# Kernel optimization log

Hardware: AMD Instinct MI355X
Metric: run time of the kernel (lower is better)

## Reference

```python
import jax, jax.numpy as jnp
import numpy as np

EMBED_DIM = 1024
B, S = 8, 2048


def setup_inputs() -> dict:
    key = jax.random.key(0)
    ks = jax.random.split(key, 8)
    scale = 1.0 / np.sqrt(EMBED_DIM)
    return {
        "mha_output": jax.random.normal(ks[0], (B, S, EMBED_DIM), dtype=jnp.float32),
        "gates": jax.random.uniform(ks[1], (B, S), dtype=jnp.float32),
        "Wq": jax.random.uniform(ks[2], (EMBED_DIM, EMBED_DIM), jnp.float32, -scale, scale),
        "bq": jax.random.uniform(ks[3], (EMBED_DIM,), jnp.float32, -scale, scale),
        "Wk": jax.random.uniform(ks[4], (EMBED_DIM, EMBED_DIM), jnp.float32, -scale, scale),
        "bk": jax.random.uniform(ks[5], (EMBED_DIM,), jnp.float32, -scale, scale),
        "Wv": jax.random.uniform(ks[6], (EMBED_DIM, EMBED_DIM), jnp.float32, -scale, scale),
        "bv": jax.random.uniform(ks[7], (EMBED_DIM,), jnp.float32, -scale, scale),
    }


def reference(mha_output, gates, Wq, bq, Wk, bk, Wv, bv):
    # gates: (B, S) -> (B, S, 1) for elementwise modulation
    g = gates[..., None]
    # Linear layers (torch convention: x @ W^T + b)
    Q = jnp.einsum('bsd,ed->bse', mha_output, Wq) + bq
    K = jnp.einsum('bsd,ed->bse', mha_output, Wk) + bk
    V = jnp.einsum('bsd,ed->bse', mha_output, Wv) + bv
    Q_mod = Q * g
    K_mod = K * g
    temperature = jnp.sqrt(jnp.asarray(EMBED_DIM, dtype=mha_output.dtype))
    scores = jnp.einsum('bqd,bkd->bqk', Q_mod, K_mod) / temperature  # (B, S, S)
    attn_weights = jax.nn.softmax(scores, axis=-1)
    gated_attn_output = jnp.einsum('bqk,bkd->bqd', attn_weights, V)
    return gated_attn_output, attn_weights
```

## Files before the change

### kernel.cpp

```cpp
#include <hip/hip_runtime.h>

#define SEQ  2048
#define EMB  1024
#define NBAT 8
#define NROW (NBAT*SEQ)

using u16 = unsigned short;
typedef float  f32x4  __attribute__((ext_vector_type(4)));
typedef __bf16 bf16x8 __attribute__((ext_vector_type(8)));
typedef u16    u16x8  __attribute__((ext_vector_type(8)));
typedef u16    u16x4  __attribute__((ext_vector_type(4)));

__device__ __forceinline__ u16 f2bf(float x) {
  unsigned u = __builtin_bit_cast(unsigned, x);
  return (u16)((u + 0x7fffu + ((u >> 16) & 1u)) >> 16);
}
__device__ __forceinline__ float bf2f(u16 h) {
  return __builtin_bit_cast(float, ((unsigned)h) << 16);
}

__device__ __forceinline__ f32x4 mfma16(u16x8 a, u16x8 b, f32x4 c) {
  return __builtin_amdgcn_mfma_f32_16x16x32_bf16(
      __builtin_bit_cast(bf16x8, a), __builtin_bit_cast(bf16x8, b), c, 0, 0, 0);
}

__device__ __forceinline__ void async_cp16(const u16* g, u16* l) {
  __builtin_amdgcn_global_load_lds(
      (const __attribute__((address_space(1))) void*)(g),
      (__attribute__((address_space(3))) void*)(l), 16, 0, 0);
}

__device__ __forceinline__ void stage_half(const u16* __restrict__ g, int ld,
                                           u16* __restrict__ lds, int wid, int lane)
{
  const int lr = lane >> 2;
  const int bb = (lr & 1) ^ ((lr >> 2) & 1);
  const int row16 = (lr & ~1) | bb;
  const int ck = (lane & 3) ^ ((lr & 2) | bb);
#pragma unroll
  for (int l = 0; l < 2; ++l) {
    const int r0 = wid * 32 + l * 16;
    async_cp16(g + (size_t)(r0 + row16) * ld + ck * 8, lds + r0 * 32);
  }
}

__device__ __forceinline__ void ph_reads_A8(const u16* __restrict__ sAh,
                                            int wr, int r, int kg, int xr, u16x8 a[8])
{
#pragma unroll
  for (int i = 0; i < 8; ++i) {
    const int row = wr * 128 + i * 16 + r;
    a[i] = *(const u16x8*)&sAh[(row * 32 + kg * 8) ^ xr];
  }
}
__device__ __forceinline__ void ph_reads_B(const u16* __restrict__ sBh,
                                           int wc, int r, int kg, int xr, u16x8 b[4])
{
#pragma unroll
  for (int j = 0; j < 4; ++j) {
    const int row = wc * 64 + j * 16 + r;
    b[j] = *(const u16x8*)&sBh[(row * 32 + kg * 8) ^ xr];
  }
}

__device__ __forceinline__ void mfma_block8(const u16x8 a[8], const u16x8 b[4],
                                            f32x4 (*accp)[4])
{
#pragma unroll
  for (int i = 0; i < 8; ++i)
#pragma unroll
    for (int j = 0; j < 4; ++j)
      accp[i][j] = mfma16(a[i], b[j], accp[i][j]);
}

#define DECL_LDS_8PH()                                                       \
  __shared__ alignas(16) u16 sAls[2][2][256 * 32];                           \
  __shared__ alignas(16) u16 sBls[2][2][256 * 32]

#define PH2(READS, STAGE, WAIT)                                              \
  READS                                                                      \
  STAGE                                                                      \
  WAIT                                                                       \
  __builtin_amdgcn_s_barrier();                                              \
  asm volatile("s_waitcnt lgkmcnt(0)" ::: "memory");                         \
  __builtin_amdgcn_sched_barrier(0);                                         \
  __builtin_amdgcn_s_setprio(1);                                             \
  mfma_block8(a_, b_, acc);                                                  \
  __builtin_amdgcn_s_setprio(0);                                             \
  __builtin_amdgcn_s_barrier();

#define GEMM_2PH(Aptr, ldA, Bptr, ldB, NTv)                                  \
  {                                                                          \
    const int r_ = lane & 15, kg_ = lane >> 4;                               \
    const int xr_ = (r_ & 7) << 3;                                           \
    stage_half((Aptr),      (ldA), &sAls[0][0][0], wid, lane);               \
    stage_half((Aptr) + 32, (ldA), &sAls[0][1][0], wid, lane);               \
    stage_half((Bptr),      (ldB), &sBls[0][0][0], wid, lane);               \
    stage_half((Bptr) + 32, (ldB), &sBls[0][1][0], wid, lane);               \
    asm volatile("s_waitcnt vmcnt(2)" ::: "memory");                         \
    __builtin_amdgcn_sched_barrier(0);                                       \
    __builtin_amdgcn_s_barrier();                                            \
    u16x8 a_[8], b_[4];                                                      \
    for (int tt = 0; tt < (NTv); ++tt) {                                     \
      const int s_ = tt & 1, s2_ = s_ ^ 1;                                   \
      const u16* A0_ = &sAls[s_][0][0]; const u16* A1_ = &sAls[s_][1][0];    \
      const u16* B0_ = &sBls[s_][0][0]; const u16* B1_ = &sBls[s_][1][0];    \
      const bool pf_ = (tt + 1 < (NTv));                                     \
      PH2({ ph_reads_A8(A0_, wr, r_, kg_, xr_, a_);                          \
            ph_reads_B(B0_, wc, r_, kg_, xr_, b_); },                        \
          { if (pf_) {                                                       \
              stage_half((Aptr) + (tt + 1) * 64,      (ldA),                 \
                         &sAls[s2_][0][0], wid, lane);                       \
              stage_half((Aptr) + (tt + 1) * 64 + 32, (ldA),                 \
                         &sAls[s2_][1][0], wid, lane);                       \
              stage_half((Bptr) + (tt + 1) * 64,      (ldB),                 \
                         &sBls[s2_][0][0], wid, lane);                       \
              stage_half((Bptr) + (tt + 1) * 64 + 32, (ldB),                 \
                         &sBls[s2_][1][0], wid, lane);                       \
            } },                                                             \
          { if (pf_) asm volatile("s_waitcnt vmcnt(8)" ::: "memory");        \
            else     asm volatile("s_waitcnt vmcnt(0)" ::: "memory");        \
            __builtin_amdgcn_sched_barrier(0); })                            \
      PH2({ ph_reads_A8(A1_, wr, r_, kg_, xr_, a_);                          \
            ph_reads_B(B1_, wc, r_, kg_, xr_, b_); },                        \
          { },                                                               \
          { if (pf_) { asm volatile("s_waitcnt vmcnt(2)" ::: "memory");      \
            __builtin_amdgcn_sched_barrier(0); } })                          \
    }                                                                        \
  }

#define DECL_ACC()                                                           \
  f32x4 acc[8][4];                                                           \
  _Pragma("unroll")                                                          \
  for (int i = 0; i < 8; ++i)                                                \
    _Pragma("unroll")                                                        \
    for (int j = 0; j < 4; ++j)                                              \
      _Pragma("unroll")                                                      \
      for (int q = 0; q < 4; ++q) acc[i][j][q] = 0.0f

__device__ __forceinline__ int xcd_swz(int bid, int nwg) {
  return (bid & 7) * (nwg >> 3) + (bid >> 3);
}

__global__ __launch_bounds__(256) void prep_kernel(
    const float* __restrict__ X,
    const float* __restrict__ Wq, const float* __restrict__ Wk, const float* __restrict__ Wv,
    u16* __restrict__ Xb, u16* __restrict__ Wb)
{
  const size_t i = ((size_t)blockIdx.x * 256 + threadIdx.x) * 4;
  const size_t nx = (size_t)NROW * EMB;
  f32x4 v;
  u16* dst;
  if (i < nx) {
    v = *(const f32x4*)(X + i);
    dst = Xb + i;
  } else {
    const size_t j = i - nx;
    const int m = (int)(j / ((size_t)EMB * EMB));
    const size_t o = j - (size_t)m * EMB * EMB;
    const float* W = (m == 0) ? Wq : (m == 1) ? Wk : Wv;
    v = *(const f32x4*)(W + o);
    dst = Wb + j;
  }
  u16x4 h;
#pragma unroll
  for (int j = 0; j < 4; ++j) h[j] = f2bf(v[j]);
  *(u16x4*)dst = h;
}

__global__ __launch_bounds__(512, 2) void proj_kernel(
    const u16* __restrict__ Xb, const u16* __restrict__ Wb,
    const float* __restrict__ bq, const float* __restrict__ bk, const float* __restrict__ bv,
    u16* __restrict__ Qb, u16* __restrict__ Kb, u16* __restrict__ VT)
{
  DECL_LDS_8PH();
  const int nwg = 4 * 64 * 3;
  int wg = xcd_swz(blockIdx.x, nwg);
  const int n0 = (wg & 3) * 256;        wg >>= 2;
  const int m0 = (wg & 63) * 256;       wg >>= 6;
  const int mat = wg;

  const int t = threadIdx.x, lane = t & 63, wid = t >> 6;
  const int wr = wid >> 2, wc = wid & 3;

  const u16* A = Xb + (size_t)m0 * EMB;
  const u16* B = Wb + (size_t)mat * EMB * EMB + (size_t)n0 * EMB;

  DECL_ACC();
  GEMM_2PH(A, EMB, B, EMB, EMB / 64);

  const float* bias = (mat == 0) ? bq : (mat == 1) ? bk : bv;
  const int r = lane & 15, kg = lane >> 4;
#pragma unroll
  for (int i = 0; i < 8; ++i) {
#pragma unroll
    for (int j = 0; j < 4; ++j) {
      const int c = n0 + wc * 64 + j * 16 + r;
      const float bb = bias[c];
      if (mat == 2) {
        const int bi = m0 >> 11;
        const int sbase = (m0 & (SEQ - 1)) + wr * 128 + i * 16 + kg * 4;
        u16x4 hv;
#pragma unroll
        for (int rg = 0; rg < 4; ++rg) hv[rg] = f2bf(acc[i][j][rg] + bb);
        *(u16x4*)&VT[((size_t)bi * EMB + c) * SEQ + sbase] = hv;
      } else {
        u16* D = (mat == 0) ? Qb : Kb;
#pragma unroll
        for (int rg = 0; rg < 4; ++rg) {
          const int row = m0 + wr * 128 + i * 16 + kg * 4 + rg;
          D[(size_t)row * EMB + c] = f2bf(acc[i][j][rg] + bb);
        }
      }
    }
  }
}

__global__ __launch_bounds__(512, 2) void scores_kernel(
    const u16* __restrict__ Qb, const u16* __restrict__ Kb,
    const float* __restrict__ gates, u16* __restrict__ raw)
{
  DECL_LDS_8PH();
  const int nwg = 8 * 8 * NBAT;
  int wg = xcd_swz(blockIdx.x, nwg);
  const int n0 = (wg & 7) * 256;        wg >>= 3;
  const int q0 = (wg & 7) * 256;        wg >>= 3;
  const int b  = wg;

  const int t = threadIdx.x, lane = t & 63, wid = t >> 6;
  const int wr = wid >> 2, wc = wid & 3;

  const u16* A = Qb + ((size_t)b * SEQ + q0) * EMB;
  const u16* B = Kb + ((size_t)b * SEQ + n0) * EMB;

  DECL_ACC();
  GEMM_2PH(A, EMB, B, EMB, EMB / 64);

  const float* gb = gates + (size_t)b * SEQ;
  u16* rawB = raw + ((size_t)b * SEQ + q0) * SEQ;
  const int r = lane & 15, kg = lane >> 4;

  float gkj[4];
#pragma unroll
  for (int j = 0; j < 4; ++j) gkj[j] = gb[n0 + wc * 64 + j * 16 + r] * 0.03125f;

#pragma unroll
  for (int i = 0; i < 8; ++i) {
#pragma unroll
    for (int rg = 0; rg < 4; ++rg) {
      const int qr = wr * 128 + i * 16 + kg * 4 + rg;
      const float gq = gb[q0 + qr];
#pragma unroll
      for (int j = 0; j < 4; ++j) {
        const int col = n0 + wc * 64 + j * 16 + r;
        rawB[(size_t)qr * SEQ + col] = f2bf(expf(acc[i][j][rg] * gq * gkj[j]));
      }
    }
  }
}

__global__ __launch_bounds__(256) void rownorm_kernel(
    const u16* __restrict__ raw, float* __restrict__ attn, float* __restrict__ invl)
{
  const int row = blockIdx.x;
  const int t = threadIdx.x, lane = t & 63, wid = t >> 6;
  const u16* rp = raw + (size_t)row * SEQ + t * 8;
  u16x8 h = *(const u16x8*)rp;
  float e[8];
  float s = 0.f;
#pragma unroll
  for (int j = 0; j < 8; ++j) { e[j] = bf2f(h[j]); s += e[j]; }
#pragma unroll
  for (int off = 32; off >= 1; off >>= 1) s += __shfl_xor(s, off);
  __shared__ float red[4];
  if (lane == 0) red[wid] = s;
  __syncthreads();
  s = (red[0] + red[1]) + (red[2] + red[3]);
  const float iv = 1.0f / s;
  float* ap = attn + (size_t)row * SEQ + t * 8;
  f32x4 w0, w1;
#pragma unroll
  for (int j = 0; j < 4; ++j) { w0[j] = e[j] * iv; w1[j] = e[j + 4] * iv; }
  *(f32x4*)ap       = w0;
  *(f32x4*)(ap + 4) = w1;
  if (t == 0) invl[row] = iv;
}

__global__ __launch_bounds__(512, 2) void pv_kernel(
    const u16* __restrict__ Eb, const u16* __restrict__ VT,
    const float* __restrict__ invl, float* __restrict__ out)
{
  DECL_LDS_8PH();
  const int nwg = 4 * 8 * NBAT;
  int wg = xcd_swz(blockIdx.x, nwg);
  const int d0 = (wg & 3) * 256;        wg >>= 2;
  const int q0 = (wg & 7) * 256;        wg >>= 3;
  const int b  = wg;

  const int t = threadIdx.x, lane = t & 63, wid = t >> 6;
  const int wr = wid >> 2, wc = wid & 3;

  const u16* A = Eb + ((size_t)b * SEQ + q0) * SEQ;
  const u16* B = VT + ((size_t)b * EMB + d0) * SEQ;

  DECL_ACC();
  GEMM_2PH(A, SEQ, B, SEQ, SEQ / 64);

  const int r = lane & 15, kg = lane >> 4;
#pragma unroll
  for (int i = 0; i < 8; ++i) {
#pragma unroll
    for (int rg = 0; rg < 4; ++rg) {
      const int rowl = q0 + wr * 128 + i * 16 + kg * 4 + rg;
      const float iv = invl[(size_t)b * SEQ + rowl];
#pragma unroll
      for (int j = 0; j < 4; ++j) {
        const int col = d0 + wc * 64 + j * 16 + r;
        out[((size_t)b * SEQ + rowl) * EMB + col] = acc[i][j][rg] * iv;
      }
    }
  }
}

extern "C" void kernel_launch(void* const* d_in, const int* in_sizes, int n_in,
                              void* d_out, int out_size, void* d_ws, size_t ws_size,
                              hipStream_t stream) {
  const float* X  = (const float*)d_in[0];
  const float* g  = (const float*)d_in[1];
  const float* Wq = (const float*)d_in[2];
  const float* bq = (const float*)d_in[3];
  const float* Wk = (const float*)d_in[4];
  const float* bk = (const float*)d_in[5];
  const float* Wv = (const float*)d_in[6];
  const float* bv = (const float*)d_in[7];

  float* out0 = (float*)d_out;
  float* attn = out0 + (size_t)NROW * EMB;

  const size_t rawN = (size_t)NBAT * SEQ * SEQ;
  const size_t need = rawN * 2 + (size_t)NBAT * EMB * SEQ * 2 + (size_t)NROW * 4;
  if (ws_size < need) return;
  u16* region0 = (u16*)d_ws;
  u16* Xb  = region0;
  u16* Wb  = region0 + (size_t)NROW * EMB;
  u16* raw = region0;
  u16* VT  = region0 + rawN;
  float* invl = (float*)(VT + (size_t)NBAT * EMB * SEQ);
  u16* Qb = (u16*)out0;
  u16* Kb = Qb + (size_t)NROW * EMB;

  const int prep_blocks = (int)(((size_t)NROW * EMB + (size_t)3 * EMB * EMB) / 1024);
  prep_kernel   <<<dim3(prep_blocks), 256, 0, stream>>>(X, Wq, Wk, Wv, Xb, Wb);
  proj_kernel   <<<dim3(768), 512, 0, stream>>>(Xb, Wb, bq, bk, bv, Qb, Kb, VT);
  scores_kernel <<<dim3(512), 512, 0, stream>>>(Qb, Kb, g, raw);
  rownorm_kernel<<<dim3(NROW), 256, 0, stream>>>(raw, attn, invl);
  pv_kernel     <<<dim3(256), 512, 0, stream>>>(raw, VT, invl, out0);
}
```

Measured before the change: 349.3 us.

## Replace double-buffered 64-K GEMM loop with triple-buffered 32-K pipeline

The shared GEMM mainloop used by the projection, scores and PV kernels changes from double-buffered 64-wide K stages with two barriers per phase to a rotating three-buffer pipeline of 32-wide K slices. Each iteration prefetches two slices ahead and keeps one barrier per step, so global loads get more time to land before the MFMAs that consume them. LDS use drops from 128KB to 96KB per block. Each MFMA block is now smaller relative to its barrier and wait overhead, and correctness depends on the vmcnt(4) accounting, which assumes each stage_half issues two loads.

```diff
diff --git a/kernel.cpp b/kernel.cpp
--- a/kernel.cpp
+++ b/kernel.cpp
@@ -73,69 +73,57 @@
       accp[i][j] = mfma16(a[i], b[j], accp[i][j]);
 }
 
-#define DECL_LDS_8PH()                                                       \
-  __shared__ alignas(16) u16 sAls[2][2][256 * 32];                           \
-  __shared__ alignas(16) u16 sBls[2][2][256 * 32]
-
-#define PH2(READS, STAGE, WAIT)                                              \
-  READS                                                                      \
-  STAGE                                                                      \
-  WAIT                                                                       \
-  __builtin_amdgcn_s_barrier();                                              \
-  asm volatile("s_waitcnt lgkmcnt(0)" ::: "memory");                         \
-  __builtin_amdgcn_sched_barrier(0);                                         \
-  __builtin_amdgcn_s_setprio(1);                                             \
-  mfma_block8(a_, b_, acc);                                                  \
-  __builtin_amdgcn_s_setprio(0);                                             \
-  __builtin_amdgcn_s_barrier();
-
-#define GEMM_2PH(Aptr, ldA, Bptr, ldB, NTv)                                  \
-  {                                                                          \
-    const int r_ = lane & 15, kg_ = lane >> 4;                               \
-    const int xr_ = (r_ & 7) << 3;                                           \
-    stage_half((Aptr),      (ldA), &sAls[0][0][0], wid, lane);               \
-    stage_half((Aptr) + 32, (ldA), &sAls[0][1][0], wid, lane);               \
-    stage_half((Bptr),      (ldB), &sBls[0][0][0], wid, lane);               \
-    stage_half((Bptr) + 32, (ldB), &sBls[0][1][0], wid, lane);               \
-    asm volatile("s_waitcnt vmcnt(2)" ::: "memory");                         \
-    __builtin_amdgcn_sched_barrier(0);                                       \
-    __builtin_amdgcn_s_barrier();                                            \
-    u16x8 a_[8], b_[4];                                                      \
-    for (int tt = 0; tt < (NTv); ++tt) {                                     \
-      const int s_ = tt & 1, s2_ = s_ ^ 1;                                   \
-      const u16* A0_ = &sAls[s_][0][0]; const u16* A1_ = &sAls[s_][1][0];    \
-      const u16* B0_ = &sBls[s_][0][0]; const u16* B1_ = &sBls[s_][1][0];    \
-      const bool pf_ = (tt + 1 < (NTv));                                     \
-      PH2({ ph_reads_A8(A0_, wr, r_, kg_, xr_, a_);                          \
-            ph_reads_B(B0_, wc, r_, kg_, xr_, b_); },                        \
-          { if (pf_) {                                                       \
-              stage_half((Aptr) + (tt + 1) * 64,      (ldA),                 \
-                         &sAls[s2_][0][0], wid, lane);                       \
-              stage_half((Aptr) + (tt + 1) * 64 + 32, (ldA),                 \
-                         &sAls[s2_][1][0], wid, lane);                       \
-              stage_half((Bptr) + (tt + 1) * 64,      (ldB),                 \
-                         &sBls[s2_][0][0], wid, lane);                       \
-              stage_half((Bptr) + (tt + 1) * 64 + 32, (ldB),                 \
-                         &sBls[s2_][1][0], wid, lane);                       \
-            } },                                                             \
-          { if (pf_) asm volatile("s_waitcnt vmcnt(8)" ::: "memory");        \
-            else     asm volatile("s_waitcnt vmcnt(0)" ::: "memory");        \
-            __builtin_amdgcn_sched_barrier(0); })                            \
-      PH2({ ph_reads_A8(A1_, wr, r_, kg_, xr_, a_);                          \
-            ph_reads_B(B1_, wc, r_, kg_, xr_, b_); },                        \
-          { },                                                               \
-          { if (pf_) { asm volatile("s_waitcnt vmcnt(2)" ::: "memory");      \
-            __builtin_amdgcn_sched_barrier(0); } })                          \
-    }                                                                        \
-  }
-
-#define DECL_ACC()                                                           \
-  f32x4 acc[8][4];                                                           \
-  _Pragma("unroll")                                                          \
-  for (int i = 0; i < 8; ++i)                                                \
-    _Pragma("unroll")                                                        \
-    for (int j = 0; j < 4; ++j)                                              \
-      _Pragma("unroll")                                                      \
+__device__ __forceinline__ void kstep256(const u16* __restrict__ sA,
+                                         const u16* __restrict__ sB,
+                                         int wr, int wc, int lane, f32x4 (*acc)[4])
+{
+  const int r = lane & 15, kg = lane >> 4;
+  const int xr = (r & 7) << 3;
+  u16x8 a[8], b[4];
+  ph_reads_B(sB, wc, r, kg, xr, b);
+  ph_reads_A8(sA, wr, r, kg, xr, a);
+  __builtin_amdgcn_s_setprio(1);
+  mfma_block8(a, b, acc);
+  __builtin_amdgcn_s_setprio(0);
+}
+
+#define GEMM_PIPE3(Aptr, ldA, Bptr, ldB, NTv)                        \
+  stage_half((Aptr), (ldA), sA0, wid, lane);                         \
+  stage_half((Bptr), (ldB), sB0, wid, lane);                         \
+  stage_half((Aptr) + 32, (ldA), sA1, wid, lane);                    \
+  stage_half((Bptr) + 32, (ldB), sB1, wid, lane);                    \
+  {                                                                  \
+    u16 *pa0 = sA0, *pa1 = sA1, *pa2 = sA2;                          \
+    u16 *pb0 = sB0, *pb1 = sB1, *pb2 = sB2;                          \
+    for (int tt = 0; tt < (NTv) - 1; ++tt) {                         \
+      asm volatile("s_waitcnt vmcnt(4)" ::: "memory");               \
+      __builtin_amdgcn_s_barrier();                                  \
+      __builtin_amdgcn_sched_barrier(0);                             \
+      if (tt + 2 < (NTv)) {                                          \
+        stage_half((Aptr) + (tt + 2) * 32, (ldA), pa2, wid, lane);   \
+        stage_half((Bptr) + (tt + 2) * 32, (ldB), pb2, wid, lane);   \
+      }                                                              \
+      kstep256(pa0, pb0, wr, wc, lane, acc);                         \
+      u16* tmp = pa0; pa0 = pa1; pa1 = pa2; pa2 = tmp;               \
+      tmp = pb0; pb0 = pb1; pb1 = pb2; pb2 = tmp;                    \
+    }                                                                \
+    asm volatile("s_waitcnt vmcnt(0)" ::: "memory");                 \
+    __builtin_amdgcn_s_barrier();                                    \
+    __builtin_amdgcn_sched_barrier(0);                               \
+    kstep256(pa0, pb0, wr, wc, lane, acc);                           \
+  }
+
+#define DECL_LDS_PIPE3()                                             \
+  __shared__ alignas(16) u16 sA0[256 * 32], sA1[256 * 32], sA2[256 * 32]; \
+  __shared__ alignas(16) u16 sB0[256 * 32], sB1[256 * 32], sB2[256 * 32]
+
+#define DECL_ACC()                                                   \
+  f32x4 acc[8][4];                                                   \
+  _Pragma("unroll")                                                  \
+  for (int i = 0; i < 8; ++i)                                        \
+    _Pragma("unroll")                                                \
+    for (int j = 0; j < 4; ++j)                                      \
+      _Pragma("unroll")                                              \
       for (int q = 0; q < 4; ++q) acc[i][j][q] = 0.0f
 
 __device__ __forceinline__ int xcd_swz(int bid, int nwg) {
@@ -173,7 +161,7 @@
     const float* __restrict__ bq, const float* __restrict__ bk, const float* __restrict__ bv,
     u16* __restrict__ Qb, u16* __restrict__ Kb, u16* __restrict__ VT)
 {
-  DECL_LDS_8PH();
+  DECL_LDS_PIPE3();
   const int nwg = 4 * 64 * 3;
   int wg = xcd_swz(blockIdx.x, nwg);
   const int n0 = (wg & 3) * 256;        wg >>= 2;
@@ -187,7 +175,7 @@
   const u16* B = Wb + (size_t)mat * EMB * EMB + (size_t)n0 * EMB;
 
   DECL_ACC();
-  GEMM_2PH(A, EMB, B, EMB, EMB / 64);
+  GEMM_PIPE3(A, EMB, B, EMB, EMB / 32);
 
   const float* bias = (mat == 0) ? bq : (mat == 1) ? bk : bv;
   const int r = lane & 15, kg = lane >> 4;
@@ -220,7 +208,7 @@
     const u16* __restrict__ Qb, const u16* __restrict__ Kb,
     const float* __restrict__ gates, u16* __restrict__ raw)
 {
-  DECL_LDS_8PH();
+  DECL_LDS_PIPE3();
   const int nwg = 8 * 8 * NBAT;
   int wg = xcd_swz(blockIdx.x, nwg);
   const int n0 = (wg & 7) * 256;        wg >>= 3;
@@ -234,7 +222,7 @@
   const u16* B = Kb + ((size_t)b * SEQ + n0) * EMB;
 
   DECL_ACC();
-  GEMM_2PH(A, EMB, B, EMB, EMB / 64);
+  GEMM_PIPE3(A, EMB, B, EMB, EMB / 32);
 
   const float* gb = gates + (size_t)b * SEQ;
   u16* rawB = raw + ((size_t)b * SEQ + q0) * SEQ;
@@ -290,7 +278,7 @@
     const u16* __restrict__ Eb, const u16* __restrict__ VT,
     const float* __restrict__ invl, float* __restrict__ out)
 {
-  DECL_LDS_8PH();
+  DECL_LDS_PIPE3();
   const int nwg = 4 * 8 * NBAT;
   int wg = xcd_swz(blockIdx.x, nwg);
   const int d0 = (wg & 3) * 256;        wg >>= 2;
@@ -304,7 +292,7 @@
   const u16* B = VT + ((size_t)b * EMB + d0) * SEQ;
 
   DECL_ACC();
-  GEMM_2PH(A, SEQ, B, SEQ, SEQ / 64);
+  GEMM_PIPE3(A, SEQ, B, SEQ, SEQ / 32);
 
   const int r = lane & 15, kg = lane >> 4;
 #pragma unroll
```

Measured after the change: 378.6 us. 1.08x slower.

## Retile projection GEMM to 128x128 blocks with three-stage LDS pipeline

Applied to the files above, without the earlier changes.

The QKV projection kernel moves from 256x256 tiles with 512 threads and a two-phase, eight-wave pipeline to 128x128 tiles with 256 threads, a K-step of 32 and a triple-buffered async LDS ring. The grid grows from 768 to 3072 blocks, which should improve occupancy and load balance across CUs, but each block reuses less data, so global traffic rises and the unswizzled LDS layout may cause bank conflicts. The scores kernel also switches expf to the fast __expf intrinsic.

```diff
diff --git a/kernel.cpp b/kernel.cpp
--- a/kernel.cpp
+++ b/kernel.cpp
@@ -30,6 +30,65 @@
       (__attribute__((address_space(3))) void*)(l), 16, 0, 0);
 }
 
+__device__ __forceinline__ int xcd_swz(int bid, int nwg) {
+  return (bid & 7) * (nwg >> 3) + (bid >> 3);
+}
+
+__device__ __forceinline__ void gload_tile128(const u16* __restrict__ g, int ld,
+                                              u16* __restrict__ lds, int wid, int lane)
+{
+#pragma unroll
+  for (int l = 0; l < 2; ++l) {
+    const int r0 = wid * 32 + l * 16;
+    const u16* src = g + (size_t)(r0 + (lane >> 2)) * ld + (lane & 3) * 8;
+    async_cp16(src, lds + r0 * 32);
+  }
+}
+
+__device__ __forceinline__ void kstep128(const u16* __restrict__ sA,
+                                         const u16* __restrict__ sB,
+                                         int wr, int wc, int lane, f32x4 acc[4][4])
+{
+  const int r = lane & 15, kg = lane >> 4;
+  u16x8 a[4], b[4];
+#pragma unroll
+  for (int i = 0; i < 4; ++i) {
+    a[i] = *(const u16x8*)&sA[(wr * 64 + i * 16 + r) * 32 + kg * 8];
+    b[i] = *(const u16x8*)&sB[(wc * 64 + i * 16 + r) * 32 + kg * 8];
+  }
+#pragma unroll
+  for (int i = 0; i < 4; ++i)
+#pragma unroll
+    for (int j = 0; j < 4; ++j)
+      acc[i][j] = mfma16(a[i], b[j], acc[i][j]);
+}
+
+#define GEMM_PIPE3_128(Aptr, ldA, Bptr, ldB, NTv)                    \
+  gload_tile128((Aptr), (ldA), sA0, wid, lane);                      \
+  gload_tile128((Bptr), (ldB), sB0, wid, lane);                      \
+  gload_tile128((Aptr) + 32, (ldA), sA1, wid, lane);                 \
+  gload_tile128((Bptr) + 32, (ldB), sB1, wid, lane);                 \
+  {                                                                  \
+    u16 *pa0 = sA0, *pa1 = sA1, *pa2 = sA2;                          \
+    u16 *pb0 = sB0, *pb1 = sB1, *pb2 = sB2;                          \
+    for (int tt = 0; tt < (NTv) - 1; ++tt) {                         \
+      asm volatile("s_waitcnt vmcnt(4)" ::: "memory");               \
+      __builtin_amdgcn_s_barrier();                                  \
+      __builtin_amdgcn_sched_barrier(0);                             \
+      if (tt + 2 < (NTv)) {                                          \
+        gload_tile128((Aptr) + (tt + 2) * 32, (ldA), pa2, wid, lane);\
+        gload_tile128((Bptr) + (tt + 2) * 32, (ldB), pb2, wid, lane);\
+      }                                                              \
+      kstep128(pa0, pb0, wr, wc, lane, acc);                         \
+      u16* tmp = pa0; pa0 = pa1; pa1 = pa2; pa2 = tmp;               \
+      tmp = pb0; pb0 = pb1; pb1 = pb2; pb2 = tmp;                    \
+    }                                                                \
+    asm volatile("s_waitcnt vmcnt(0)" ::: "memory");                 \
+    __builtin_amdgcn_s_barrier();                                    \
+    __builtin_amdgcn_sched_barrier(0);                               \
+    kstep128(pa0, pb0, wr, wc, lane, acc);                           \
+  }
+
 __device__ __forceinline__ void stage_half(const u16* __restrict__ g, int ld,
                                            u16* __restrict__ lds, int wid, int lane)
 {
@@ -73,7 +132,7 @@
       accp[i][j] = mfma16(a[i], b[j], accp[i][j]);
 }
 
-#define DECL_LDS_8PH()                                                       \
+#define DECL_LDS_2PH()                                                       \
   __shared__ alignas(16) u16 sAls[2][2][256 * 32];                           \
   __shared__ alignas(16) u16 sBls[2][2][256 * 32]
 
@@ -129,18 +188,14 @@
     }                                                                        \
   }
 
-#define DECL_ACC()                                                           \
-  f32x4 acc[8][4];                                                           \
-  _Pragma("unroll")                                                          \
-  for (int i = 0; i < 8; ++i)                                                \
-    _Pragma("unroll")                                                        \
-    for (int j = 0; j < 4; ++j)                                              \
-      _Pragma("unroll")                                                      \
+#define DECL_ACC84()                                                 \
+  f32x4 acc[8][4];                                                   \
+  _Pragma("unroll")                                                  \
+  for (int i = 0; i < 8; ++i)                                        \
+    _Pragma("unroll")                                                \
+    for (int j = 0; j < 4; ++j)                                      \
+      _Pragma("unroll")                                              \
       for (int q = 0; q < 4; ++q) acc[i][j][q] = 0.0f
-
-__device__ __forceinline__ int xcd_swz(int bid, int nwg) {
-  return (bid & 7) * (nwg >> 3) + (bid >> 3);
-}
 
 __global__ __launch_bounds__(256) void prep_kernel(
     const float* __restrict__ X,
@@ -168,38 +223,47 @@
   *(u16x4*)dst = h;
 }
 
-__global__ __launch_bounds__(512, 2) void proj_kernel(
+__global__ __launch_bounds__(256) void proj_kernel(
     const u16* __restrict__ Xb, const u16* __restrict__ Wb,
     const float* __restrict__ bq, const float* __restrict__ bk, const float* __restrict__ bv,
     u16* __restrict__ Qb, u16* __restrict__ Kb, u16* __restrict__ VT)
 {
-  DECL_LDS_8PH();
-  const int nwg = 4 * 64 * 3;
+  __shared__ alignas(16) u16 sA0[128 * 32], sA1[128 * 32], sA2[128 * 32];
+  __shared__ alignas(16) u16 sB0[128 * 32], sB1[128 * 32], sB2[128 * 32];
+
+  const int nwg = (EMB / 128) * (NROW / 128) * 3;
   int wg = xcd_swz(blockIdx.x, nwg);
-  const int n0 = (wg & 3) * 256;        wg >>= 2;
-  const int m0 = (wg & 63) * 256;       wg >>= 6;
+  const int n0 = (wg & 7) * 128;        wg >>= 3;
+  const int m0 = (wg & 127) * 128;      wg >>= 7;
   const int mat = wg;
 
   const int t = threadIdx.x, lane = t & 63, wid = t >> 6;
-  const int wr = wid >> 2, wc = wid & 3;
+  const int wr = wid >> 1, wc = wid & 1;
 
   const u16* A = Xb + (size_t)m0 * EMB;
   const u16* B = Wb + (size_t)mat * EMB * EMB + (size_t)n0 * EMB;
 
-  DECL_ACC();
-  GEMM_2PH(A, EMB, B, EMB, EMB / 64);
+  f32x4 acc[4][4];
+#pragma unroll
+  for (int i = 0; i < 4; ++i)
+#pragma unroll
+    for (int j = 0; j < 4; ++j)
+#pragma unroll
+      for (int q = 0; q < 4; ++q) acc[i][j][q] = 0.0f;
+
+  GEMM_PIPE3_128(A, EMB, B, EMB, EMB / 32);
 
   const float* bias = (mat == 0) ? bq : (mat == 1) ? bk : bv;
   const int r = lane & 15, kg = lane >> 4;
 #pragma unroll
-  for (int i = 0; i < 8; ++i) {
+  for (int i = 0; i < 4; ++i) {
 #pragma unroll
     for (int j = 0; j < 4; ++j) {
       const int c = n0 + wc * 64 + j * 16 + r;
       const float bb = bias[c];
       if (mat == 2) {
         const int bi = m0 >> 11;
-        const int sbase = (m0 & (SEQ - 1)) + wr * 128 + i * 16 + kg * 4;
+        const int sbase = (m0 & (SEQ - 1)) + wr * 64 + i * 16 + kg * 4;
         u16x4 hv;
 #pragma unroll
         for (int rg = 0; rg < 4; ++rg) hv[rg] = f2bf(acc[i][j][rg] + bb);
@@ -208,7 +272,7 @@
         u16* D = (mat == 0) ? Qb : Kb;
 #pragma unroll
         for (int rg = 0; rg < 4; ++rg) {
-          const int row = m0 + wr * 128 + i * 16 + kg * 4 + rg;
+          const int row = m0 + wr * 64 + i * 16 + kg * 4 + rg;
           D[(size_t)row * EMB + c] = f2bf(acc[i][j][rg] + bb);
         }
       }
@@ -220,7 +284,7 @@
     const u16* __restrict__ Qb, const u16* __restrict__ Kb,
     const float* __restrict__ gates, u16* __restrict__ raw)
 {
-  DECL_LDS_8PH();
+  DECL_LDS_2PH();
   const int nwg = 8 * 8 * NBAT;
   int wg = xcd_swz(blockIdx.x, nwg);
   const int n0 = (wg & 7) * 256;        wg >>= 3;
@@ -233,7 +297,7 @@
   const u16* A = Qb + ((size_t)b * SEQ + q0) * EMB;
   const u16* B = Kb + ((size_t)b * SEQ + n0) * EMB;
 
-  DECL_ACC();
+  DECL_ACC84();
   GEMM_2PH(A, EMB, B, EMB, EMB / 64);
 
   const float* gb = gates + (size_t)b * SEQ;
@@ -253,7 +317,7 @@
 #pragma unroll
       for (int j = 0; j < 4; ++j) {
         const int col = n0 + wc * 64 + j * 16 + r;
-        rawB[(size_t)qr * SEQ + col] = f2bf(expf(acc[i][j][rg] * gq * gkj[j]));
+        rawB[(size_t)qr * SEQ + col] = f2bf(__expf(acc[i][j][rg] * gq * gkj[j]));
       }
     }
   }
@@ -290,7 +354,7 @@
     const u16* __restrict__ Eb, const u16* __restrict__ VT,
     const float* __restrict__ invl, float* __restrict__ out)
 {
-  DECL_LDS_8PH();
+  DECL_LDS_2PH();
   const int nwg = 4 * 8 * NBAT;
   int wg = xcd_swz(blockIdx.x, nwg);
   const int d0 = (wg & 3) * 256;        wg >>= 2;
@@ -303,7 +367,7 @@
   const u16* A = Eb + ((size_t)b * SEQ + q0) * SEQ;
   const u16* B = VT + ((size_t)b * EMB + d0) * SEQ;
 
-  DECL_ACC();
+  DECL_ACC84();
   GEMM_2PH(A, SEQ, B, SEQ, SEQ / 64);
 
   const int r = lane & 15, kg = lane >> 4;
@@ -351,7 +415,7 @@
 
   const int prep_blocks = (int)(((size_t)NROW * EMB + (size_t)3 * EMB * EMB) / 1024);
   prep_kernel   <<<dim3(prep_blocks), 256, 0, stream>>>(X, Wq, Wk, Wv, Xb, Wb);
-  proj_kernel   <<<dim3(768), 512, 0, stream>>>(Xb, Wb, bq, bk, bv, Qb, Kb, VT);
+  proj_kernel   <<<dim3(3072), 256, 0, stream>>>(Xb, Wb, bq, bk, bv, Qb, Kb, VT);
   scores_kernel <<<dim3(512), 512, 0, stream>>>(Qb, Kb, g, raw);
   rownorm_kernel<<<dim3(NROW), 256, 0, stream>>>(raw, attn, invl);
   pv_kernel     <<<dim3(256), 512, 0, stream>>>(raw, VT, invl, out0);
```

New measurement: 354.2 us. About the same (+1.4%).
